# Kernel tuning notes

Hardware: AMD Instinct MI355X
Metric: run time of the kernel (lower is better)

The kernel has to match this reference:

```python
import jax, jax.numpy as jnp
import numpy as np

# ---- constants from SystemsOfSprings.f ----
TS = 0.05                      # integration step h
K_G, C_G = 1.0, 2.0            # ground spring / damper (k1..k4, c1..c4)
K_I, C_I = 1.0, 0.0            # inter-agent spring / damper (k5..k10, c5..c10)
_L9 = float(np.sqrt(4.0 ** 2 + 1.5 ** 2))
EDGE_I = jnp.array([0, 1, 2, 3, 2, 3])          # springs 5,6,7,8,9,10
EDGE_J = jnp.array([1, 2, 3, 0, 0, 1])
EDGE_L = jnp.array([4.0, 1.5, 4.0, 1.5, _L9, _L9], dtype=jnp.float32)
XBAR = jnp.array([2.0, 2.0, 0.0, 0.0, -2.0, 2.0, 0.0, 0.0,
                  -2.0, -2.0, 0.0, 0.0, 2.0, -2.0, 0.0, 0.0], dtype=jnp.float32)


def _step(x, u, xbar):
    # x: (16,) = [px,py,vx,vy] x 4 agents; u: (8,) = 2 force inputs per agent
    px, py, vx, vy = x[0::4], x[1::4], x[2::4], x[3::4]      # (4,) each (Mx/My/Mvx/Mvy selections)
    xt, yt = xbar[0::4], xbar[1::4]

    # ground spring + damper forces (toward target, opposing velocity)
    dxt, dyt = px - xt, py - yt
    ang_t = jnp.arctan2(dyt, dxt)
    ang_v = jnp.arctan2(vy, vx)
    Fk0 = K_G * jnp.sqrt(dxt ** 2 + dyt ** 2)
    Fc0 = C_G * jnp.sqrt(vx ** 2 + vy ** 2)
    Fgx = -Fk0 * jnp.cos(ang_t) - Fc0 * jnp.cos(ang_v)
    Fgy = -Fk0 * jnp.sin(ang_t) - Fc0 * jnp.sin(ang_v)

    # inter-agent springs/dampers on the 6 edges (edge list, no 4x4 diagonal NaNs)
    dxe = px[EDGE_I] - px[EDGE_J]
    dye = py[EDGE_I] - py[EDGE_J]
    dvxe = vx[EDGE_I] - vx[EDGE_J]
    dvye = vy[EDGE_I] - vy[EDGE_J]
    Fke = K_I * (jnp.sqrt(dxe ** 2 + dye ** 2) - EDGE_L)
    Fce = C_I * jnp.sqrt(dvxe ** 2 + dvye ** 2)
    ang = jnp.arctan2(dye, dxe)      # angle from j toward i's perspective at i
    angv = jnp.arctan2(dvye, dvxe)
    cxe, sye = jnp.cos(ang), jnp.sin(ang)
    cve, sve = jnp.cos(angv), jnp.sin(angv)
    # force on agent i: -F*proj(i,j); on agent j: -F*proj(j,i) = +F*proj(i,j)
    z4 = jnp.zeros(4, x.dtype)
    Fsx = z4.at[EDGE_I].add(-Fke * cxe).at[EDGE_J].add(Fke * cxe)
    Fsy = z4.at[EDGE_I].add(-Fke * sye).at[EDGE_J].add(Fke * sye)
    Fdx = z4.at[EDGE_I].add(-Fce * cve).at[EDGE_J].add(Fce * cve)
    Fdy = z4.at[EDGE_I].add(-Fce * sve).at[EDGE_J].add(Fce * sve)

    accx = Fsx + Fdx + Fgx  # masses m1..m4 = 1
    accy = Fsy + Fdy + Fgy

    dx = jnp.zeros(16, x.dtype)
    dx = dx.at[0::4].set(vx).at[1::4].set(vy).at[2::4].set(accx).at[3::4].set(accy)
    Bu = jnp.zeros(16, x.dtype).at[2::4].set(u[0::2]).at[3::4].set(u[1::2])
    return x + (dx + Bu) * TS


def setup_inputs() -> dict:
    key = jax.random.key(0)
    kx, ku = jax.random.split(key)
    B = 1048576
    x = jax.random.normal(kx, (B, 16), dtype=jnp.float32)
    u = jax.random.normal(ku, (B, 8), dtype=jnp.float32)
    return {"t": 0, "x": x, "u": u, "w": jnp.zeros((16,), jnp.float32), "xbar": XBAR}


def reference(t, x, u, w, xbar):
    # t and w are unused, exactly as in the torch forward; batch via vmap
    return jax.vmap(lambda xi, ui: _step(xi, ui, xbar))(x, u)
```

## Files before the change

### kernel.cpp

```cpp
#include <hip/hip_runtime.h>
#include <math.h>


#define TS 0.05f

__global__ __launch_bounds__(256) void springs_node_kernel(
    const float* __restrict__ x,
    const float* __restrict__ u,
    float* __restrict__ out,
    int N)
{
    int g = blockIdx.x * blockDim.x + threadIdx.x;
    if (g >= N) return;

    int node = g & 3;

    float4 s  = reinterpret_cast<const float4*>(x)[g];
    float2 uc = reinterpret_cast<const float2*>(u)[g];

    float px = s.x, py = s.y, vx = s.z, vy = s.w;

    float xt = (node == 1 || node == 2) ? -2.f : 2.f;
    float yt = (node >= 2) ? -2.f : 2.f;

    float ax = -(px - xt) - 2.f * vx;
    float ay = -(py - yt) - 2.f * vy;

    const float Ld[3] = { 4.0f, 4.2720018727f , 1.5f };

#pragma unroll
    for (int d = 1; d <= 3; ++d) {
        float qx = __shfl_xor(px, d, 64);
        float qy = __shfl_xor(py, d, 64);
        float dx = px - qx;
        float dy = py - qy;
        float d2 = dx * dx + dy * dy;
        float L  = Ld[d - 1];

        float r    = sqrtf(d2);
        bool  nz   = (d2 > 0.f);
        float invr = nz ? (1.f / r) : 0.f;
        float c    = nz ? (dx * invr) : 1.f;
        float sn   = dy * invr;
        float Fk   = r - L;

        ax -= Fk * c;
        ay -= Fk * sn;
    }

    float4 r4;
    r4.x = px + TS * vx;
    r4.y = py + TS * vy;
    r4.z = vx + TS * (ax + uc.x);
    r4.w = vy + TS * (ay + uc.y);

    reinterpret_cast<float4*>(out)[g] = r4;
}

extern "C" void kernel_launch(void* const* d_in, const int* in_sizes, int n_in,
                              void* d_out, int out_size, void* d_ws, size_t ws_size,
                              hipStream_t stream) {
    const float* x = (const float*)d_in[1];
    const float* u = (const float*)d_in[2];
    float* out = (float*)d_out;

    int N = in_sizes[1] / 4;
    int block = 256;
    int grid = (N + block - 1) / block;
    springs_node_kernel<<<grid, block, 0, stream>>>(x, u, out, N);
}
```

Baseline: 145.6 us.

## Process four elements per thread with DPP quad permutes and rsqrt edge forces

Each thread now handles four strided float4 elements, issuing all loads before computing, which raises memory-level parallelism and cuts the grid size. Neighbor exchange inside each 4-lane agent group uses DPP quad_perm instead of ds_bpermute-style shuffles. The spring force is computed with a single hardware reciprocal square root and FMAs, where before it used a sqrt followed by a divide. The kernel is memory-bound, so the main gain expected comes from load batching, at the cost of slightly lower rsqrt precision.

```diff
diff --git a/kernel.cpp b/kernel.cpp
--- a/kernel.cpp
+++ b/kernel.cpp
@@ -1,8 +1,28 @@
 #include <hip/hip_runtime.h>
-#include <math.h>
 
 
 #define TS 0.05f
+#define NELEM 4
+
+template<int CTRL>
+__device__ __forceinline__ float qp(float v) {
+    return __int_as_float(__builtin_amdgcn_update_dpp(
+        0, __float_as_int(v), CTRL, 0xF, 0xF, true));
+}
+
+__device__ __forceinline__ void edge(float px, float py, float qx, float qy,
+                                     float L, float& ax, float& ay) {
+    float dx = px - qx;
+    float dy = py - qy;
+    float d2 = fmaf(dx, dx, dy * dy);
+    float invr = __builtin_amdgcn_rsqf(d2);
+    float s = fmaf(-L, invr, 1.0f);
+    bool nz = d2 > 0.f;
+    float fx = nz ? dx * s : -L;
+    float fy = nz ? dy * s : 0.f;
+    ax -= fx;
+    ay -= fy;
+}
 
 __global__ __launch_bounds__(256) void springs_node_kernel(
     const float* __restrict__ x,
@@ -10,51 +30,53 @@
     float* __restrict__ out,
     int N)
 {
-    int g = blockIdx.x * blockDim.x + threadIdx.x;
-    if (g >= N) return;
+    const int t = threadIdx.x;
+    const int base = blockIdx.x * (256 * NELEM) + t;
+    const int node = t & 3;
 
-    int node = g & 3;
+    const float xt = (node == 1 || node == 2) ? -2.f : 2.f;
+    const float yt = (node >= 2) ? -2.f : 2.f;
 
-    float4 s  = reinterpret_cast<const float4*>(x)[g];
-    float2 uc = reinterpret_cast<const float2*>(u)[g];
+    const float4* x4 = reinterpret_cast<const float4*>(x);
+    const float2* u2 = reinterpret_cast<const float2*>(u);
+    float4*       o4 = reinterpret_cast<float4*>(out);
 
-    float px = s.x, py = s.y, vx = s.z, vy = s.w;
-
-    float xt = (node == 1 || node == 2) ? -2.f : 2.f;
-    float yt = (node >= 2) ? -2.f : 2.f;
-
-    float ax = -(px - xt) - 2.f * vx;
-    float ay = -(py - yt) - 2.f * vy;
-
-    const float Ld[3] = { 4.0f, 4.2720018727f , 1.5f };
+    float4 s[NELEM];
+    float2 uc[NELEM];
+    bool   ok[NELEM];
 
 #pragma unroll
-    for (int d = 1; d <= 3; ++d) {
-        float qx = __shfl_xor(px, d, 64);
-        float qy = __shfl_xor(py, d, 64);
-        float dx = px - qx;
-        float dy = py - qy;
-        float d2 = dx * dx + dy * dy;
-        float L  = Ld[d - 1];
-
-        float r    = sqrtf(d2);
-        bool  nz   = (d2 > 0.f);
-        float invr = nz ? (1.f / r) : 0.f;
-        float c    = nz ? (dx * invr) : 1.f;
-        float sn   = dy * invr;
-        float Fk   = r - L;
-
-        ax -= Fk * c;
-        ay -= Fk * sn;
+    for (int e = 0; e < NELEM; ++e) {
+        int g = base + e * 256;
+        ok[e] = (g < N);
+        if (ok[e]) {
+            s[e]  = x4[g];
+            uc[e] = u2[g];
+        }
     }
 
-    float4 r4;
-    r4.x = px + TS * vx;
-    r4.y = py + TS * vy;
-    r4.z = vx + TS * (ax + uc.x);
-    r4.w = vy + TS * (ay + uc.y);
+#pragma unroll
+    for (int e = 0; e < NELEM; ++e) {
+        float px = s[e].x, py = s[e].y, vx = s[e].z, vy = s[e].w;
 
-    reinterpret_cast<float4*>(out)[g] = r4;
+        float ax = -(px - xt) - 2.f * vx;
+        float ay = -(py - yt) - 2.f * vy;
+
+        edge(px, py, qp<0xB1>(px), qp<0xB1>(py), 4.0f,          ax, ay);
+        edge(px, py, qp<0x4E>(px), qp<0x4E>(py), 4.2720018727f, ax, ay);
+        edge(px, py, qp<0x1B>(px), qp<0x1B>(py), 1.5f,          ax, ay);
+
+        float4 r;
+        r.x = fmaf(TS, vx, px);
+        r.y = fmaf(TS, vy, py);
+        r.z = fmaf(TS, ax + uc[e].x, vx);
+        r.w = fmaf(TS, ay + uc[e].y, vy);
+
+        if (ok[e]) {
+            int g = base + e * 256;
+            o4[g] = r;
+        }
+    }
 }
 
 extern "C" void kernel_launch(void* const* d_in, const int* in_sizes, int n_in,
@@ -65,7 +87,7 @@
     float* out = (float*)d_out;
 
     int N = in_sizes[1] / 4;
-    int block = 256;
-    int grid = (N + block - 1) / block;
-    springs_node_kernel<<<grid, block, 0, stream>>>(x, u, out, N);
+    int per_block = 256 * NELEM;
+    int grid = (N + per_block - 1) / per_block;
+    springs_node_kernel<<<grid, 256, 0, stream>>>(x, u, out, N);
 }
```

Result: no change. 147.9 us (+1.6%).
